# Performance work log

Measured on AMD Instinct MI355X. Metric: run time of the kernel, lower is better.

## Reference

```python
import jax, jax.numpy as jnp
import numpy as np

N = 4096
IN_F = 128
OUT_F = 64      # per-head out_features
HEADS = 4
ALPHA = 0.2     # LeakyReLU negative slope
NEG_FILL = -9e15


def setup_inputs() -> dict:
    key = jax.random.key(0)
    k_h, k_adj, k_W, k_a = jax.random.split(key, 4)
    h = jax.random.normal(k_h, (N, IN_F), dtype=jnp.float32)
    adj = jax.random.randint(k_adj, (N, N), 0, 2, dtype=jnp.int32)
    W = jax.random.normal(k_W, (IN_F, OUT_F * HEADS), dtype=jnp.float32) * 0.1
    a = jax.random.normal(k_a, (2 * OUT_F, 1), dtype=jnp.float32) * 0.1
    bias = jnp.zeros((OUT_F * HEADS,), dtype=jnp.float32)
    return {"h": h, "adj": adj, "W": W, "a": a, "bias": bias}


def reference(h, adj, W, a, bias):
    n = h.shape[0]
    Wh = (h @ W).reshape(n, HEADS, OUT_F)            # (N, H, F)
    # e_ij = leakyrelu(a_left . Wh_i + a_right . Wh_j)  (decomposed outer sum;
    # same math as concat([Wh_i, Wh_j]) @ a in the original)
    a_left = a[:OUT_F, 0]                            # (F,)
    a_right = a[OUT_F:, 0]                           # (F,)
    left = jnp.einsum('nhf,f->nh', Wh, a_left)       # (N, H)
    right = jnp.einsum('nhf,f->nh', Wh, a_right)     # (N, H)
    mask = adj > 0                                   # (N, N)
    outs = []
    for head in range(HEADS):                        # small fixed loop over heads
        e = left[:, head, None] + right[None, :, head]          # (N, N)
        e = jnp.where(e >= 0, e, ALPHA * e)                      # LeakyReLU
        e = jnp.where(mask, e, NEG_FILL)
        attn = jax.nn.softmax(e, axis=1)                         # (N, N)
        outs.append(attn @ Wh[:, head, :])                       # (N, F)
    out = jnp.concatenate(outs, axis=1)              # concat=True -> (N, H*F)
    return out + bias
```

## Files before the change

kernel.cpp:

```cpp
#include <hip/hip_runtime.h>
#include <hip/hip_bf16.h>

#define NN 4096
#define IN_F 128
#define OUT_F 64
#define C_TOT 256
#define ALPHA 0.2f
#define LOG2E 1.4426950408889634f

typedef float f32x4 __attribute__((ext_vector_type(4)));
typedef __bf16 bf16x8 __attribute__((ext_vector_type(8)));

__device__ __forceinline__ unsigned fmap(float f) {
    unsigned u = __float_as_uint(f);
    return (u >> 31) ? ~u : (u | 0x80000000u);
}
__device__ __forceinline__ float funmap(unsigned u) {
    return (u >> 31) ? __uint_as_float(u & 0x7FFFFFFFu) : __uint_as_float(~u);
}
__device__ __forceinline__ unsigned short bfbits(float x) {
    union { __bf16 b; unsigned short u; } t;
    t.b = (__bf16)x;
    return t.u;
}
__device__ __forceinline__ void gl16(const void* g, void* l) {
    __builtin_amdgcn_global_load_lds((const __attribute__((address_space(1))) void*)g,
                                     (__attribute__((address_space(3))) void*)l, 16, 0, 0);
}

__global__ __launch_bounds__(256) void k_misc(
    const float* __restrict__ W, const float* __restrict__ a,
    unsigned short* __restrict__ WTbf, float* __restrict__ uLR,
    unsigned int* __restrict__ Rmax)
{
    const int b = blockIdx.x, tid = threadIdx.x;
    const int c = b * 8 + (tid & 7);
#pragma unroll
    for (int pass = 0; pass < 4; ++pass) {
        const int k = pass * 32 + (tid >> 3);
        WTbf[(size_t)c * IN_F + k] = bfbits(W[k * C_TOT + c]);
    }
    if (b == 0) {
        if (tid < 4) Rmax[tid] = 0u;
        for (int o = tid; o < 1024; o += 256) {
            const int k = o >> 3, j = o & 7;
            const int hd = j & 3, side = j >> 2;
            float s = 0.f;
            for (int f = 0; f < OUT_F; ++f)
                s = fmaf(W[k * C_TOT + hd * OUT_F + f], a[side * OUT_F + f], s);
            uLR[k * 8 + side * 4 + hd] = s;
        }
    }
}

__global__ __launch_bounds__(256) void k_mask(
    const int* __restrict__ adj, unsigned* __restrict__ mask)
{
    const int lane = threadIdx.x & 63, wv = threadIdx.x >> 6;
    const int row = blockIdx.x * 4 + wv;
    const int* __restrict__ ar = adj + (size_t)row * NN;
    unsigned* __restrict__ mr = mask + (size_t)row * 128;
    for (int c = 0; c < 8; ++c) {
        const int j0 = c * 512;
        unsigned w = 0u;
#pragma unroll
        for (int k = 0; k < 8; ++k) {
            const unsigned long long bb = __ballot(ar[j0 + k * 64 + lane] > 0);
            const unsigned lo = (unsigned)bb, hi = (unsigned)(bb >> 32);
            if ((lane >> 1) == k) w = (lane & 1) ? hi : lo;
        }
        if (lane < 16) mr[(j0 >> 5) + lane] = w;
    }
}

__global__ __launch_bounds__(256) void k_prep(
    const float* __restrict__ hmat, const unsigned short* __restrict__ WTbf,
    const float* __restrict__ uLR, unsigned short* __restrict__ WhT,
    float* __restrict__ leftT, float* __restrict__ rightT,
    unsigned int* __restrict__ Rmax)
{
    __shared__ float hs[16][132];
    __shared__ float us[128][8];
    const int tid = threadIdx.x;
    const int rowbase = blockIdx.x * 16;

    ((float4*)us)[tid] = ((const float4*)uLR)[tid];
#pragma unroll
    for (int p = 0; p < 8; ++p) {
        const int idx = p * 256 + tid;
        hs[idx >> 7][idx & 127] = hmat[(size_t)rowbase * IN_F + idx];
    }
    __syncthreads();

    const int lane = tid & 63, wv = tid >> 6;
    const int m16 = lane & 15, kg = lane >> 4;

    if (wv == 0) {
        const int row = lane >> 2, hd = lane & 3;
        float aL = 0.f, aR = 0.f;
#pragma unroll
        for (int k = 0; k < 128; k += 4) {
            const float4 hv = *(const float4*)&hs[row][k];
            aL = fmaf(hv.x, us[k][hd],   fmaf(hv.y, us[k+1][hd],   fmaf(hv.z, us[k+2][hd],   fmaf(hv.w, us[k+3][hd],   aL))));
            aR = fmaf(hv.x, us[k][hd+4], fmaf(hv.y, us[k+1][hd+4], fmaf(hv.z, us[k+2][hd+4], fmaf(hv.w, us[k+3][hd+4], aR))));
        }
        leftT [hd * NN + rowbase + row] = aL;
        rightT[hd * NN + rowbase + row] = aR * LOG2E;
        float mx = aR;
#pragma unroll
        for (int s = 4; s < 64; s <<= 1) mx = fmaxf(mx, __shfl_xor(mx, s, 64));
        if (lane < 4) atomicMax(&Rmax[hd], fmap(mx));
    }

    bf16x8 afr[4];
#pragma unroll
    for (int ks = 0; ks < 4; ++ks) {
        const float4 lo = *(const float4*)&hs[m16][ks * 32 + kg * 8];
        const float4 hi = *(const float4*)&hs[m16][ks * 32 + kg * 8 + 4];
        bf16x8 v;
        v[0] = (__bf16)lo.x; v[1] = (__bf16)lo.y; v[2] = (__bf16)lo.z; v[3] = (__bf16)lo.w;
        v[4] = (__bf16)hi.x; v[5] = (__bf16)hi.y; v[6] = (__bf16)hi.z; v[7] = (__bf16)hi.w;
        afr[ks] = v;
    }

#pragma unroll
    for (int nt0 = 0; nt0 < 4; ++nt0) {
        const int col = (wv * 4 + nt0) * 16 + m16;
        f32x4 acc = (f32x4){0.f, 0.f, 0.f, 0.f};
#pragma unroll
        for (int ks = 0; ks < 4; ++ks) {
            union { uint4 u; bf16x8 v; } B;
            B.u = *(const uint4*)(WTbf + (size_t)col * IN_F + ks * 32 + kg * 8);
            acc = __builtin_amdgcn_mfma_f32_16x16x32_bf16(afr[ks], B.v, acc, 0, 0, 0);
        }
#pragma unroll
        for (int i = 0; i < 4; ++i)
            WhT[(size_t)col * NN + rowbase + kg * 4 + i] = bfbits(acc[i]);
    }
}

__global__ __launch_bounds__(512, 4) void k_attn(
    const unsigned* __restrict__ mask,
    const unsigned short* __restrict__ WhT,
    const float* __restrict__ leftT,
    const float* __restrict__ rightT,
    const unsigned int* __restrict__ Rmax,
    const float* __restrict__ bias,
    float* __restrict__ out)
{
    __shared__ unsigned short Bb[2][64 * 128];
    __shared__ float rlds[4096];
    __shared__ unsigned mask_lds[32 * 132];

    const int tid = threadIdx.x;
    const int lane = tid & 63;
    const int wv = tid >> 6;
    const int rh = wv & 1;
    const int j4 = wv >> 1;
    const int rowbase = (blockIdx.x >> 2) * 32;
    const int hd = blockIdx.x & 3;
    const int m = lane & 15;
    const int kg = lane >> 4;
    const int sh = kg * 8;

#pragma unroll
    for (int p = 0; p < 2; ++p) {
        const int i = p * 512 + tid;
        const uint4 v = *(const uint4*)(mask + (size_t)(rowbase + (i >> 5)) * 128 + (i & 31) * 4);
        *(uint4*)&mask_lds[(i >> 5) * 132 + (i & 31) * 4] = v;
    }
#pragma unroll
    for (int p = 0; p < 2; ++p) {
        const int i = p * 512 + tid;
        *(float4*)&rlds[i * 4] = *(const float4*)(rightT + (size_t)hd * NN + i * 4);
    }

    const float lf = leftT[hd * NN + rowbase + rh * 16 + m];
    const float rmx = funmap(Rmax[hd]);
    const float x = lf + rmx;
    const float m0v = fmaxf(x, ALPHA * x);
    const float mp0 = m0v * LOG2E;
    const float lf2 = fmaf(lf, LOG2E, -mp0);
    const float qc = -0.8f * mp0;

    __syncthreads();

    const int srow0 = wv * 4 + (lane >> 4);
    const int g_lin = lane & 15;
    const int lg = g_lin ^ (srow0 & 15);
    const unsigned short* gsrc0 = WhT + (size_t)(hd * 64 + srow0) * NN + lg * 8;
    const unsigned short* gsrc1 = gsrc0 + (size_t)32 * NN;
    const int d0 = wv * 512 + lane * 8;

#define STAGE(buf, t) {                                  \
    gl16(gsrc0 + (t) * 128, &Bb[buf][d0]);               \
    gl16(gsrc1 + (t) * 128, &Bb[buf][4096 + d0]); }

    const int pg8 = ((j4 * 4 + kg) ^ m) * 8;
    const int bro = m * 128 + pg8;

    f32x4 acc0 = (f32x4){0,0,0,0}, acc1 = acc0, acc2 = acc0, acc3 = acc0;
    float lpart = 0.f;
    const int mrow_off = (rh * 16 + m) * 132;

#define COMPUTE(buf, t) {                                                        \
    const unsigned aw = mask_lds[mrow_off + (t) * 4 + j4] >> sh;                 \
    const float4 ra  = *(const float4*)&rlds[(t) * 128 + j4 * 32 + sh];          \
    const float4 rb4 = *(const float4*)&rlds[(t) * 128 + j4 * 32 + sh + 4];      \
    const float rv[8] = { ra.x, ra.y, ra.z, ra.w, rb4.x, rb4.y, rb4.z, rb4.w };  \
    union { __bf16 b[8]; bf16x8 v; } Af;                                         \
    _Pragma("unroll")                                                            \
    for (int i = 0; i < 8; ++i) {                                                \
        const float p = rv[i] + lf2;                                             \
        const float q = fmaf(p, ALPHA, qc);                                      \
        const float t2 = fmaxf(p, q);                                            \
        float w = exp2f(t2);                                                     \
        const unsigned mk = (unsigned)(((int)(aw << (31 - i))) >> 31);           \
        w = __uint_as_float(__float_as_uint(w) & mk);                            \
        lpart += w;                                                              \
        Af.b[i] = (__bf16)w;                                                     \
    }                                                                            \
    union { uint4 u; bf16x8 v; } B0, B1, B2, B3;                                 \
    B0.u = *(const uint4*)&Bb[buf][bro];                                         \
    B1.u = *(const uint4*)&Bb[buf][bro + 2048];                                  \
    B2.u = *(const uint4*)&Bb[buf][bro + 4096];                                  \
    B3.u = *(const uint4*)&Bb[buf][bro + 6144];                                  \
    acc0 = __builtin_amdgcn_mfma_f32_16x16x32_bf16(Af.v, B0.v, acc0, 0, 0, 0);   \
    acc1 = __builtin_amdgcn_mfma_f32_16x16x32_bf16(Af.v, B1.v, acc1, 0, 0, 0);   \
    acc2 = __builtin_amdgcn_mfma_f32_16x16x32_bf16(Af.v, B2.v, acc2, 0, 0, 0);   \
    acc3 = __builtin_amdgcn_mfma_f32_16x16x32_bf16(Af.v, B3.v, acc3, 0, 0, 0);   \
}

    STAGE(0, 0);
    for (int t = 0; t < 31; ++t) {
        STAGE((t + 1) & 1, t + 1);
        asm volatile("s_waitcnt vmcnt(2)" ::: "memory");
        __builtin_amdgcn_sched_barrier(0);
        __builtin_amdgcn_s_barrier();
        COMPUTE(t & 1, t);
        __builtin_amdgcn_sched_barrier(0);
        __builtin_amdgcn_s_barrier();
    }
    asm volatile("s_waitcnt vmcnt(0)" ::: "memory");
    __builtin_amdgcn_sched_barrier(0);
    __builtin_amdgcn_s_barrier();
    COMPUTE(1, 31);
#undef STAGE
#undef COMPUTE

    __syncthreads();
    float* comb = (float*)&Bb[0][0];
    if (j4 > 0) {
        float* c = comb + (((j4 - 1) * 2 + rh) * 64 + lane) * 17;
#pragma unroll
        for (int i = 0; i < 4; ++i) {
            c[ 0 + i] = acc0[i]; c[ 4 + i] = acc1[i];
            c[ 8 + i] = acc2[i]; c[12 + i] = acc3[i];
        }
        c[16] = lpart;
    }
    __syncthreads();
    if (j4 == 0) {
#pragma unroll
        for (int pt = 0; pt < 3; ++pt) {
            const float* c = comb + ((pt * 2 + rh) * 64 + lane) * 17;
#pragma unroll
            for (int i = 0; i < 4; ++i) {
                acc0[i] += c[ 0 + i]; acc1[i] += c[ 4 + i];
                acc2[i] += c[ 8 + i]; acc3[i] += c[12 + i];
            }
            lpart += c[16];
        }
        float lsum = lpart;
        lsum += __shfl_xor(lsum, 16, 64);
        lsum += __shfl_xor(lsum, 32, 64);

#pragma unroll
        for (int q = 0; q < 4; ++q) {
            const f32x4 A = (q == 0) ? acc0 : (q == 1) ? acc1 : (q == 2) ? acc2 : acc3;
            const int col = hd * 64 + q * 16 + m;
            const float bv = bias[col];
#pragma unroll
            for (int i = 0; i < 4; ++i) {
                const int r = kg * 4 + i;
                const float lr = __shfl(lsum, r, 64);
                out[(size_t)(rowbase + rh * 16 + r) * C_TOT + col] = A[i] / lr + bv;
            }
        }
    }
}

extern "C" void kernel_launch(void* const* d_in, const int* in_sizes, int n_in,
                              void* d_out, int out_size, void* d_ws, size_t ws_size,
                              hipStream_t stream) {
    const float* hmat = (const float*)d_in[0];
    const int*   adj  = (const int*)d_in[1];
    const float* W    = (const float*)d_in[2];
    const float* a    = (const float*)d_in[3];
    const float* bias = (const float*)d_in[4];
    float* out = (float*)d_out;

    char* ws = (char*)d_ws;
    unsigned short* WhT  = (unsigned short*)(ws + 0x000000);
    float* rightT        = (float*)(ws + 0x280000);
    float* leftT         = (float*)(ws + 0x2A0000);
    unsigned short* WTbf = (unsigned short*)(ws + 0x2B0000);
    float* uLR           = (float*)(ws + 0x2C0000);
    unsigned int* Rmax   = (unsigned int*)(ws + 0x2C1000);
    unsigned* mask       = (unsigned*)(ws + 0x300000);

    hipLaunchKernelGGL(k_misc, dim3(32),   dim3(256), 0, stream, W, a, WTbf, uLR, Rmax);
    hipLaunchKernelGGL(k_mask, dim3(1024), dim3(256), 0, stream, adj, mask);
    hipLaunchKernelGGL(k_prep, dim3(256),  dim3(256), 0, stream, hmat, WTbf, uLR, WhT, leftT, rightT, Rmax);
    hipLaunchKernelGGL(k_attn, dim3(512),  dim3(512), 0, stream, mask, WhT, leftT, rightT, Rmax, bias, out);
}
```

Baseline: 72.36 us.

## Deepen attention pipeline to 4 LDS buffers, keep mask in registers, fuse prep kernels

The attention kernel now uses a 4-deep LDS ring for WhT tiles with prefetch distance 2 and a single barrier per iteration, cutting one barrier each step and leaving more latency slack for loads. The bitmask is stored in a transposed layout so each thread loads its 32 mask words straight into registers, which removes the mask LDS staging. The small W-transpose/uLR kernel is folded into the mask kernel to save one launch. These changes add register pressure and LDS footprint, and the single-barrier ring depends on correct buffer-reuse distance.

```diff
diff --git a/kernel.cpp b/kernel.cpp
--- a/kernel.cpp
+++ b/kernel.cpp
@@ -28,35 +28,14 @@
                                      (__attribute__((address_space(3))) void*)l, 16, 0, 0);
 }
 
-__global__ __launch_bounds__(256) void k_misc(
+__global__ __launch_bounds__(256) void k_mask(
+    const int* __restrict__ adj, unsigned* __restrict__ mask,
     const float* __restrict__ W, const float* __restrict__ a,
     unsigned short* __restrict__ WTbf, float* __restrict__ uLR,
     unsigned int* __restrict__ Rmax)
 {
-    const int b = blockIdx.x, tid = threadIdx.x;
-    const int c = b * 8 + (tid & 7);
-#pragma unroll
-    for (int pass = 0; pass < 4; ++pass) {
-        const int k = pass * 32 + (tid >> 3);
-        WTbf[(size_t)c * IN_F + k] = bfbits(W[k * C_TOT + c]);
-    }
-    if (b == 0) {
-        if (tid < 4) Rmax[tid] = 0u;
-        for (int o = tid; o < 1024; o += 256) {
-            const int k = o >> 3, j = o & 7;
-            const int hd = j & 3, side = j >> 2;
-            float s = 0.f;
-            for (int f = 0; f < OUT_F; ++f)
-                s = fmaf(W[k * C_TOT + hd * OUT_F + f], a[side * OUT_F + f], s);
-            uLR[k * 8 + side * 4 + hd] = s;
-        }
-    }
-}
-
-__global__ __launch_bounds__(256) void k_mask(
-    const int* __restrict__ adj, unsigned* __restrict__ mask)
-{
-    const int lane = threadIdx.x & 63, wv = threadIdx.x >> 6;
+    const int tid = threadIdx.x;
+    const int lane = tid & 63, wv = tid >> 6;
     const int row = blockIdx.x * 4 + wv;
     const int* __restrict__ ar = adj + (size_t)row * NN;
     unsigned* __restrict__ mr = mask + (size_t)row * 128;
@@ -69,7 +48,31 @@
             const unsigned lo = (unsigned)bb, hi = (unsigned)(bb >> 32);
             if ((lane >> 1) == k) w = (lane & 1) ? hi : lo;
         }
-        if (lane < 16) mr[(j0 >> 5) + lane] = w;
+        if (lane < 16) {
+            const int wi = c * 16 + lane;
+            mr[(wi & 3) * 32 + (wi >> 2)] = w;
+        }
+    }
+
+    if (blockIdx.x < 32) {
+        const int b = blockIdx.x;
+        const int c = b * 8 + (tid & 7);
+#pragma unroll
+        for (int pass = 0; pass < 4; ++pass) {
+            const int k = pass * 32 + (tid >> 3);
+            WTbf[(size_t)c * IN_F + k] = bfbits(W[k * C_TOT + c]);
+        }
+        if (b == 0) {
+            if (tid < 4) Rmax[tid] = 0u;
+            for (int o = tid; o < 1024; o += 256) {
+                const int k = o >> 3, j = o & 7;
+                const int hd = j & 3, side = j >> 2;
+                float s = 0.f;
+                for (int f = 0; f < OUT_F; ++f)
+                    s = fmaf(W[k * C_TOT + hd * OUT_F + f], a[side * OUT_F + f], s);
+                uLR[k * 8 + side * 4 + hd] = s;
+            }
+        }
     }
 }
 
@@ -148,9 +151,8 @@
     const float* __restrict__ bias,
     float* __restrict__ out)
 {
-    __shared__ unsigned short Bb[2][64 * 128];
+    __shared__ unsigned short Bb[4][64 * 128];
     __shared__ float rlds[4096];
-    __shared__ unsigned mask_lds[32 * 132];
 
     const int tid = threadIdx.x;
     const int lane = tid & 63;
@@ -166,13 +168,17 @@
 #pragma unroll
     for (int p = 0; p < 2; ++p) {
         const int i = p * 512 + tid;
-        const uint4 v = *(const uint4*)(mask + (size_t)(rowbase + (i >> 5)) * 128 + (i & 31) * 4);
-        *(uint4*)&mask_lds[(i >> 5) * 132 + (i & 31) * 4] = v;
-    }
-#pragma unroll
-    for (int p = 0; p < 2; ++p) {
-        const int i = p * 512 + tid;
         *(float4*)&rlds[i * 4] = *(const float4*)(rightT + (size_t)hd * NN + i * 4);
+    }
+    unsigned mreg[32];
+    {
+        const unsigned* mrow = mask + (size_t)(rowbase + rh * 16 + m) * 128 + j4 * 32;
+#pragma unroll
+        for (int p = 0; p < 8; ++p) {
+            const uint4 v = *(const uint4*)(mrow + p * 4);
+            mreg[p * 4 + 0] = v.x; mreg[p * 4 + 1] = v.y;
+            mreg[p * 4 + 2] = v.z; mreg[p * 4 + 3] = v.w;
+        }
     }
 
     const float lf = leftT[hd * NN + rowbase + rh * 16 + m];
@@ -201,10 +207,9 @@
 
     f32x4 acc0 = (f32x4){0,0,0,0}, acc1 = acc0, acc2 = acc0, acc3 = acc0;
     float lpart = 0.f;
-    const int mrow_off = (rh * 16 + m) * 132;
 
 #define COMPUTE(buf, t) {                                                        \
-    const unsigned aw = mask_lds[mrow_off + (t) * 4 + j4] >> sh;                 \
+    const unsigned aw = mreg[(t)] >> sh;                                         \
     const float4 ra  = *(const float4*)&rlds[(t) * 128 + j4 * 32 + sh];          \
     const float4 rb4 = *(const float4*)&rlds[(t) * 128 + j4 * 32 + sh + 4];      \
     const float rv[8] = { ra.x, ra.y, ra.z, ra.w, rb4.x, rb4.y, rb4.z, rb4.w };  \
@@ -232,19 +237,18 @@
 }
 
     STAGE(0, 0);
-    for (int t = 0; t < 31; ++t) {
-        STAGE((t + 1) & 1, t + 1);
-        asm volatile("s_waitcnt vmcnt(2)" ::: "memory");
+    STAGE(1, 1);
+#pragma unroll
+    for (int t = 0; t < 32; ++t) {
+        if (t + 2 < 32) STAGE((t + 2) & 3, t + 2);
+        if (t < 30)       { asm volatile("s_waitcnt vmcnt(4)" ::: "memory"); }
+        else if (t == 30) { asm volatile("s_waitcnt vmcnt(2)" ::: "memory"); }
+        else              { asm volatile("s_waitcnt vmcnt(0)" ::: "memory"); }
         __builtin_amdgcn_sched_barrier(0);
         __builtin_amdgcn_s_barrier();
-        COMPUTE(t & 1, t);
         __builtin_amdgcn_sched_barrier(0);
-        __builtin_amdgcn_s_barrier();
-    }
-    asm volatile("s_waitcnt vmcnt(0)" ::: "memory");
-    __builtin_amdgcn_sched_barrier(0);
-    __builtin_amdgcn_s_barrier();
-    COMPUTE(1, 31);
+        COMPUTE(t & 3, t);
+    }
 #undef STAGE
 #undef COMPUTE
 
@@ -309,8 +313,10 @@
     unsigned int* Rmax   = (unsigned int*)(ws + 0x2C1000);
     unsigned* mask       = (unsigned*)(ws + 0x300000);
 
-    hipLaunchKernelGGL(k_misc, dim3(32),   dim3(256), 0, stream, W, a, WTbf, uLR, Rmax);
-    hipLaunchKernelGGL(k_mask, dim3(1024), dim3(256), 0, stream, adj, mask);
-    hipLaunchKernelGGL(k_prep, dim3(256),  dim3(256), 0, stream, hmat, WTbf, uLR, WhT, leftT, rightT, Rmax);
-    hipLaunchKernelGGL(k_attn, dim3(512),  dim3(512), 0, stream, mask, WhT, leftT, rightT, Rmax, bias, out);
-}
+    hipLaunchKernelGGL(k_mask, dim3(1024), dim3(256), 0, stream,
+                       adj, mask, W, a, WTbf, uLR, Rmax);
+    hipLaunchKernelGGL(k_prep, dim3(256),  dim3(256), 0, stream,
+                       hmat, WTbf, uLR, WhT, leftT, rightT, Rmax);
+    hipLaunchKernelGGL(k_attn, dim3(512),  dim3(512), 0, stream,
+                       mask, WhT, leftT, rightT, Rmax, bias, out);
+}
```

Result: faster. 69.24 us (-4.3%).
